# Performance work log

Hardware: AMD Instinct MI355X
Metric: run time of the kernel (lower is better)

## Reference

```python
import jax, jax.numpy as jnp
import numpy as np

T = 8192   # sequence length (= max_seq_len)
E = 1024   # embedding dim
D = 11     # hard-coded projection dim in source


def setup_inputs() -> dict:
    key = jax.random.key(0)
    ks = jax.random.split(key, 6)
    s_e = 1.0 / np.sqrt(E)
    s_d = 1.0 / np.sqrt(D)
    return {
        "x": jax.random.randint(ks[0], (T,), 0, 32000, dtype=jnp.int64),
        "x_embeddings": jax.random.normal(ks[1], (T, E), dtype=jnp.float32),
        "Wk": jax.random.normal(ks[2], (D, E), dtype=jnp.float32) * s_e,
        "bk": jnp.zeros((D,), dtype=jnp.float32),
        "Wq": jax.random.normal(ks[3], (D, E), dtype=jnp.float32) * s_e,
        "bq": jnp.zeros((D,), dtype=jnp.float32),
        "Wv": jax.random.normal(ks[4], (D, E), dtype=jnp.float32) * s_e,
        "bv": jnp.zeros((D,), dtype=jnp.float32),
        "Wf": jax.random.normal(ks[5], (E, D), dtype=jnp.float32) * s_d,
        "bf": jnp.zeros((E,), dtype=jnp.float32),
    }


def reference(x, x_embeddings, Wk, bk, Wq, bq, Wv, bv, Wf, bf):
    t = x.shape[0]  # static under jit
    k = x_embeddings @ Wk.T + bk            # [T, D]
    q = x_embeddings @ Wq.T + bq            # [T, D]
    v = x_embeddings @ Wv.T + bv            # [T, D]
    att = q @ k.T                           # [T, T]; NOTE: no 1/sqrt(D) scaling in source
    causal = jnp.tril(jnp.ones((t, t), dtype=bool))
    att = jnp.where(causal, att, -jnp.inf)
    att = jax.nn.softmax(att, axis=1)       # dim=1 as in source
    res = att @ v                           # [T, D]
    return res @ Wf.T + bf                  # [T, E]
```

## Files before the change

kernel.cpp:

```cpp
#include <hip/hip_runtime.h>

#define T_SEQ 8192
#define E_DIM 1024
#define QS 36
#define NEC 8
#define ECOLS 128
#define NC4 32
#define X4ST 33
#define RB 64
#define RPB 512
#define NIB (T_SEQ / RPB)
#define KVW 24
#define TR 16
#define LOG2E 1.4426950408889634f

__device__ __forceinline__ float2 pkfma(float2 a, float2 b, float2 c) {
    return make_float2(fmaf(a.x, b.x, c.x), fmaf(a.y, b.y, c.y));
}
__device__ __forceinline__ float2 f2(float x, float y) { return make_float2(x, y); }


__global__ __launch_bounds__(256) void prep_wf(const float* __restrict__ Wf,
                                               float* __restrict__ Wfp) {
    int id = blockIdx.x * 256 + threadIdx.x;
    if (id >= E_DIM * 12) return;
    int e = id / 12, d = id % 12;
    Wfp[id] = (d < 11) ? Wf[(size_t)e * 11 + d] : 0.f;
}

__global__ __launch_bounds__(256) void qkv_proj(
    const float* __restrict__ xe,
    const float* __restrict__ Wk, const float* __restrict__ bk,
    const float* __restrict__ Wq, const float* __restrict__ bq,
    const float* __restrict__ Wv, const float* __restrict__ bv,
    float* __restrict__ partQ) {
    const int row0 = blockIdx.x * RB;
    const int ec = blockIdx.y;
    const int lane = threadIdx.x & 63;
    const int wg = threadIdx.x >> 6;
    const int cb = ec * ECOLS;

    __shared__ float4 xT[RB * X4ST];
    __shared__ float4 wT[36 * NC4];

#pragma unroll
    for (int t = 0; t < 8; ++t) {
        int idx = threadIdx.x + t * 256;
        int r = idx >> 5, c4 = idx & 31;
        xT[r * X4ST + c4] =
            *(const float4*)(xe + (size_t)(row0 + r) * E_DIM + cb + c4 * 4);
    }
    for (int idx = threadIdx.x; idx < 36 * NC4; idx += 256) {
        int r = idx >> 5, c4 = idx & 31;
        float4 v = make_float4(0.f, 0.f, 0.f, 0.f);
        if (r < 33) {
            const float* base = (r < 11) ? (Wk + (size_t)r * E_DIM)
                              : (r < 22) ? (Wq + (size_t)(r - 11) * E_DIM)
                                         : (Wv + (size_t)(r - 22) * E_DIM);
            v = *(const float4*)(base + cb + c4 * 4);
        }
        wT[idx] = v;
    }
    __syncthreads();

    float2 acc[9];
#pragma unroll
    for (int k = 0; k < 9; ++k) acc[k] = f2(0.f, 0.f);

    const float4* xr = xT + lane * X4ST;
    const float4* wr = wT + wg * 9 * NC4;
#pragma unroll 4
    for (int c4 = 0; c4 < NC4; ++c4) {
        float4 xv = xr[c4];
        float2 xlo = f2(xv.x, xv.y), xhi = f2(xv.z, xv.w);
#pragma unroll
        for (int k = 0; k < 9; ++k) {
            float4 wv = wr[k * NC4 + c4];
            acc[k] = pkfma(xlo, f2(wv.x, wv.y), acc[k]);
            acc[k] = pkfma(xhi, f2(wv.z, wv.w), acc[k]);
        }
    }

    float* dst = partQ + ((size_t)ec * T_SEQ + row0 + lane) * QS;
#pragma unroll
    for (int k = 0; k < 9; ++k) {
        int o = wg * 9 + k;
        bool live = (o < 33);
        int c = (o < 11) ? o : (o < 22) ? o + 1 : (o < 33) ? o + 2
                : (o == 33) ? 11 : (o == 34) ? 23 : 35;
        float b = 0.f;
        if (ec == 0 && live)
            b = (o < 11) ? bk[o] : (o < 22) ? bq[o - 11] : bv[o - 22];
        dst[c] = live ? (acc[k].x + acc[k].y + b) : 0.f;
    }
}

__global__ __launch_bounds__(256) void reduceQ(const float* __restrict__ partQ,
                                               float* __restrict__ qkvF) {
    const size_t idx = (size_t)blockIdx.x * 256 + threadIdx.x;
    const float4* p = (const float4*)partQ;
    const size_t cs = (size_t)T_SEQ * (QS / 4);
    float4 s = make_float4(0.f, 0.f, 0.f, 0.f);
#pragma unroll
    for (int c = 0; c < NEC; ++c) {
        float4 a = p[idx + (size_t)c * cs];
        s.x += a.x; s.y += a.y; s.z += a.z; s.w += a.w;
    }
    ((float4*)qkvF)[idx] = s;
}

template <int LJCH>
__device__ __forceinline__ void stage_kv(const float* __restrict__ qkvF,
                                         float* kv, int j0) {
    for (int idx = threadIdx.x; idx < LJCH * 6; idx += 256) {
        int row = idx / 6, f = idx % 6;
        int srcOff = f * 4 + (f >= 3 ? 12 : 0);
        float4 v = *(const float4*)(qkvF + (size_t)(j0 + row) * QS + srcOff);
        *(float4*)(kv + row * KVW + f * 4) = v;
    }
}

template <int LJCH>
__device__ __forceinline__ void attn_chunk(const float* kv, int j0, int r0,
    const float4& qa0, const float4& qa1, const float4& qa2,
    const float4& qb0, const float4& qb1, const float4& qb2,
    float2& a01, float2& a23, float2& a45, float2& a67, float2& a89, float2& aXL,
    float2& b01, float2& b23, float2& b45, float2& b67, float2& b89, float2& bXL) {
#pragma unroll 2
    for (int jj = 0; jj < LJCH; ++jj) {
        const float* kp = kv + jj * KVW;
        const float4 kA = *(const float4*)(kp);
        const float4 kB = *(const float4*)(kp + 4);
        const float4 kC = *(const float4*)(kp + 8);
        const float4 vA = *(const float4*)(kp + 12);
        const float4 vB = *(const float4*)(kp + 16);
        const float4 vC = *(const float4*)(kp + 20);

        float2 sa = pkfma(f2(qa0.x, qa0.y), f2(kA.x, kA.y),
                    pkfma(f2(qa0.z, qa0.w), f2(kA.z, kA.w),
                    pkfma(f2(qa1.x, qa1.y), f2(kB.x, kB.y),
                    pkfma(f2(qa1.z, qa1.w), f2(kB.z, kB.w),
                    pkfma(f2(qa2.x, qa2.y), f2(kC.x, kC.y), f2(0.f, 0.f))))));
        float2 sb = pkfma(f2(qb0.x, qb0.y), f2(kA.x, kA.y),
                    pkfma(f2(qb0.z, qb0.w), f2(kA.z, kA.w),
                    pkfma(f2(qb1.x, qb1.y), f2(kB.x, kB.y),
                    pkfma(f2(qb1.z, qb1.w), f2(kB.z, kB.w),
                    pkfma(f2(qb2.x, qb2.y), f2(kC.x, kC.y), f2(0.f, 0.f))))));
        float pa = exp2f(sa.x + sa.y + qa2.z * kC.z);
        float pb = exp2f(sb.x + sb.y + qb2.z * kC.z);
        const int j = j0 + jj;
        pa = (j <= r0)     ? pa : 0.f;
        pb = (j <= r0 + 1) ? pb : 0.f;
        float2 pa2 = f2(pa, pa), pb2 = f2(pb, pb);
        a01 = pkfma(pa2, f2(vA.x, vA.y), a01);
        a23 = pkfma(pa2, f2(vA.z, vA.w), a23);
        a45 = pkfma(pa2, f2(vB.x, vB.y), a45);
        a67 = pkfma(pa2, f2(vB.z, vB.w), a67);
        a89 = pkfma(pa2, f2(vC.x, vC.y), a89);
        aXL = pkfma(pa2, f2(vC.z, 1.f),  aXL);
        b01 = pkfma(pb2, f2(vA.x, vA.y), b01);
        b23 = pkfma(pb2, f2(vA.z, vA.w), b23);
        b45 = pkfma(pb2, f2(vB.x, vB.y), b45);
        b67 = pkfma(pb2, f2(vB.z, vB.w), b67);
        b89 = pkfma(pb2, f2(vC.x, vC.y), b89);
        bXL = pkfma(pb2, f2(vC.z, 1.f),  bXL);
    }
}

template <int LJCH, int H>
__global__ __launch_bounds__(256, 4) void attn(const float* __restrict__ qkvF,
                                               float* __restrict__ part) {
    const int b = blockIdx.x;
    int ib = (int)((sqrtf((float)(8 * b / H + 1)) - 1.0f) * 0.5f);
    while (H * (ib + 1) * (ib + 2) / 2 <= b) ++ib;
    while (H * ib * (ib + 1) / 2 > b) --ib;
    const int s = b - H * ib * (ib + 1) / 2;
    const int chunkB = 2 * H * (ib + 1) - 1 - s;

    const int row0 = ib * RPB;
    const int r0 = row0 + threadIdx.x * 2;

    const float* qp0 = qkvF + (size_t)r0 * QS + 12;
    const float* qp1 = qp0 + QS;
    float4 qa0 = *(const float4*)(qp0), qa1 = *(const float4*)(qp0 + 4), qa2 = *(const float4*)(qp0 + 8);
    float4 qb0 = *(const float4*)(qp1), qb1 = *(const float4*)(qp1 + 4), qb2 = *(const float4*)(qp1 + 8);
    qa0.x *= LOG2E; qa0.y *= LOG2E; qa0.z *= LOG2E; qa0.w *= LOG2E;
    qa1.x *= LOG2E; qa1.y *= LOG2E; qa1.z *= LOG2E; qa1.w *= LOG2E;
    qa2.x *= LOG2E; qa2.y *= LOG2E; qa2.z *= LOG2E;
    qb0.x *= LOG2E; qb0.y *= LOG2E; qb0.z *= LOG2E; qb0.w *= LOG2E;
    qb1.x *= LOG2E; qb1.y *= LOG2E; qb1.z *= LOG2E; qb1.w *= LOG2E;
    qb2.x *= LOG2E; qb2.y *= LOG2E; qb2.z *= LOG2E;

    float2 a01 = f2(0.f, 0.f), a23 = a01, a45 = a01, a67 = a01, a89 = a01, aXL = a01;
    float2 b01 = a01, b23 = a01, b45 = a01, b67 = a01, b89 = a01, bXL = a01;

    __shared__ float kv[LJCH * KVW];

#pragma unroll
    for (int pass = 0; pass < 2; ++pass) {
        const int jc = pass ? chunkB : s;
        const int j0 = jc * LJCH;
        if (pass) __syncthreads();
        stage_kv<LJCH>(qkvF, kv, j0);
        __syncthreads();
        attn_chunk<LJCH>(kv, j0, r0, qa0, qa1, qa2, qb0, qb1, qb2,
                         a01, a23, a45, a67, a89, aXL, b01, b23, b45, b67, b89, bXL);
    }

    float* dst = part + ((size_t)s * T_SEQ + r0) * 12;
    float4 t;
    t.x = a01.x; t.y = a01.y; t.z = a23.x; t.w = a23.y; *(float4*)(dst + 0)  = t;
    t.x = a45.x; t.y = a45.y; t.z = a67.x; t.w = a67.y; *(float4*)(dst + 4)  = t;
    t.x = a89.x; t.y = a89.y; t.z = aXL.x; t.w = aXL.y; *(float4*)(dst + 8)  = t;
    t.x = b01.x; t.y = b01.y; t.z = b23.x; t.w = b23.y; *(float4*)(dst + 12) = t;
    t.x = b45.x; t.y = b45.y; t.z = b67.x; t.w = b67.y; *(float4*)(dst + 16) = t;
    t.x = b89.x; t.y = b89.y; t.z = bXL.x; t.w = bXL.y; *(float4*)(dst + 20) = t;
}

__global__ __launch_bounds__(256) void pass2(const float* __restrict__ part,
                                             const float* __restrict__ Wfp,
                                             const float* __restrict__ bf,
                                             float* __restrict__ out, int H) {
    const int t0 = blockIdx.x * TR;
    __shared__ float res[TR][12];
    const int cnt = H * (t0 / RPB) + H;
    if (threadIdx.x < TR * 12) {
        const float* p = part + (size_t)t0 * 12 + threadIdx.x;
        const size_t S = (size_t)T_SEQ * 12;
        float v[4];
#pragma unroll
        for (int u = 0; u < 4; ++u) v[u] = 0.f;
        for (int c = 0; c < cnt; c += 4) {
#pragma unroll
            for (int u = 0; u < 4; ++u) v[u] += p[(size_t)(c + u) * S];
        }
        float sum = (v[0] + v[1]) + (v[2] + v[3]);
        const int d = threadIdx.x % 12;
        res[threadIdx.x / 12][d] = (d == 11) ? (1.f / sum) : sum;
    }
    __syncthreads();

    const int e0 = threadIdx.x * 4;
    float4 wf[4][3];
#pragma unroll
    for (int ee = 0; ee < 4; ++ee) {
        const float4* wp = (const float4*)(Wfp + (size_t)(e0 + ee) * 12);
        wf[ee][0] = wp[0]; wf[ee][1] = wp[1]; wf[ee][2] = wp[2];
    }
    const float4 bv = *(const float4*)(bf + e0);

    for (int r = 0; r < TR; ++r) {
        float rr[12];
#pragma unroll
        for (int d = 0; d < 12; ++d) rr[d] = res[r][d];
        float2 a0 = f2(0.f, 0.f), a1 = a0, a2 = a0, a3 = a0;
#pragma unroll
        for (int d = 0; d < 10; d += 2) {
            float2 rv = f2(rr[d], rr[d + 1]);
            a0 = pkfma(rv, f2(((const float*)&wf[0][0])[d], ((const float*)&wf[0][0])[d + 1]), a0);
            a1 = pkfma(rv, f2(((const float*)&wf[1][0])[d], ((const float*)&wf[1][0])[d + 1]), a1);
            a2 = pkfma(rv, f2(((const float*)&wf[2][0])[d], ((const float*)&wf[2][0])[d + 1]), a2);
            a3 = pkfma(rv, f2(((const float*)&wf[3][0])[d], ((const float*)&wf[3][0])[d + 1]), a3);
        }
        const float rl = rr[11];
        float4 ov;
        ov.x = (a0.x + a0.y + rr[10] * wf[0][2].z) * rl + bv.x;
        ov.y = (a1.x + a1.y + rr[10] * wf[1][2].z) * rl + bv.y;
        ov.z = (a2.x + a2.y + rr[10] * wf[2][2].z) * rl + bv.z;
        ov.w = (a3.x + a3.y + rr[10] * wf[3][2].z) * rl + bv.w;
        *(float4*)(out + (size_t)(t0 + r) * E_DIM + e0) = ov;
    }
}

extern "C" void kernel_launch(void* const* d_in, const int* in_sizes, int n_in,
                              void* d_out, int out_size, void* d_ws, size_t ws_size,
                              hipStream_t stream) {
    const float* xe = (const float*)d_in[1];
    const float* Wk = (const float*)d_in[2];
    const float* bk = (const float*)d_in[3];
    const float* Wq = (const float*)d_in[4];
    const float* bq = (const float*)d_in[5];
    const float* Wv = (const float*)d_in[6];
    const float* bv = (const float*)d_in[7];
    const float* Wf = (const float*)d_in[8];
    const float* bf = (const float*)d_in[9];
    float* out = (float*)d_out;

    float* qkvF  = (float*)d_ws;
    float* wfp   = qkvF + (size_t)T_SEQ * QS;
    float* partQ = wfp + (size_t)E_DIM * 12;
    float* part  = partQ;

    const size_t fixed = ((size_t)T_SEQ * QS + (size_t)E_DIM * 12) * 4;
    const size_t need32 = fixed + (size_t)128 * T_SEQ * 12 * 4;

    prep_wf<<<(E_DIM * 12 + 255) / 256, 256, 0, stream>>>(Wf, wfp);
    qkv_proj<<<dim3(T_SEQ / RB, NEC), 256, 0, stream>>>(xe, Wk, bk, Wq, bq, Wv, bv, partQ);
    reduceQ<<<(T_SEQ * (QS / 4)) / 256, 256, 0, stream>>>(partQ, qkvF);

    if (ws_size >= need32) {
        attn<32, 8><<<8 * NIB * (NIB + 1) / 2, 256, 0, stream>>>(qkvF, part);
        pass2<<<T_SEQ / TR, 256, 0, stream>>>(part, wfp, bf, out, 8);
    } else {
        attn<64, 4><<<4 * NIB * (NIB + 1) / 2, 256, 0, stream>>>(qkvF, part);
        pass2<<<T_SEQ / TR, 256, 0, stream>>>(part, wfp, bf, out, 4);
    }
}
```

Measured before the change: 194.0 us.

## Register-block four rows per thread in QKV projection and causal attention

The QKV projection now has each thread compute four rows against a 64-column slice, using 16 column chunks. This reuses each shared-memory weight load across four rows. The attention kernel moves to 1024-row blocks with four query rows per thread and 64-key chunks, which reuses each K/V shared load four times, and it pads the kv stride. In exchange it uses more registers (launch bounds drop to 2 blocks per SM), launches fewer blocks, and removes the workspace-size fallback path.

```diff
diff --git a/kernel.cpp b/kernel.cpp
--- a/kernel.cpp
+++ b/kernel.cpp
@@ -3,14 +3,15 @@
 #define T_SEQ 8192
 #define E_DIM 1024
 #define QS 36
-#define NEC 8
-#define ECOLS 128
-#define NC4 32
-#define X4ST 33
-#define RB 64
-#define RPB 512
-#define NIB (T_SEQ / RPB)
-#define KVW 24
+#define QNEC 16
+#define QKC 64
+#define QX4 16
+#define QXST 17
+#define QRB 256
+#define AJC 64
+#define ARB 1024
+#define ANIB (T_SEQ / ARB)
+#define KVW 32
 #define TR 16
 #define LOG2E 1.4426950408889634f
 
@@ -28,30 +29,30 @@
     Wfp[id] = (d < 11) ? Wf[(size_t)e * 11 + d] : 0.f;
 }
 
-__global__ __launch_bounds__(256) void qkv_proj(
+__global__ __launch_bounds__(256, 2) void qkv_proj(
     const float* __restrict__ xe,
     const float* __restrict__ Wk, const float* __restrict__ bk,
     const float* __restrict__ Wq, const float* __restrict__ bq,
     const float* __restrict__ Wv, const float* __restrict__ bv,
     float* __restrict__ partQ) {
-    const int row0 = blockIdx.x * RB;
+    const int row0 = blockIdx.x * QRB;
     const int ec = blockIdx.y;
     const int lane = threadIdx.x & 63;
     const int wg = threadIdx.x >> 6;
-    const int cb = ec * ECOLS;
-
-    __shared__ float4 xT[RB * X4ST];
-    __shared__ float4 wT[36 * NC4];
-
-#pragma unroll
-    for (int t = 0; t < 8; ++t) {
+    const int cb = ec * QKC;
+
+    __shared__ float4 xT[QRB * QXST];
+    __shared__ float4 wT[36 * QX4];
+
+#pragma unroll
+    for (int t = 0; t < 16; ++t) {
         int idx = threadIdx.x + t * 256;
-        int r = idx >> 5, c4 = idx & 31;
-        xT[r * X4ST + c4] =
+        int r = idx >> 4, c4 = idx & 15;
+        xT[r * QXST + c4] =
             *(const float4*)(xe + (size_t)(row0 + r) * E_DIM + cb + c4 * 4);
     }
-    for (int idx = threadIdx.x; idx < 36 * NC4; idx += 256) {
-        int r = idx >> 5, c4 = idx & 31;
+    for (int idx = threadIdx.x; idx < 36 * QX4; idx += 256) {
+        int r = idx >> 4, c4 = idx & 15;
         float4 v = make_float4(0.f, 0.f, 0.f, 0.f);
         if (r < 33) {
             const float* base = (r < 11) ? (Wk + (size_t)r * E_DIM)
@@ -63,21 +64,32 @@
     }
     __syncthreads();
 
-    float2 acc[9];
-#pragma unroll
-    for (int k = 0; k < 9; ++k) acc[k] = f2(0.f, 0.f);
-
-    const float4* xr = xT + lane * X4ST;
-    const float4* wr = wT + wg * 9 * NC4;
+    float2 acc[4][9];
+#pragma unroll
+    for (int u = 0; u < 4; ++u)
+#pragma unroll
+        for (int k = 0; k < 9; ++k) acc[u][k] = f2(0.f, 0.f);
+
+    const float4* xr = xT + lane * QXST;
+    const float4* wr = wT + wg * 9 * QX4;
 #pragma unroll 4
-    for (int c4 = 0; c4 < NC4; ++c4) {
-        float4 xv = xr[c4];
-        float2 xlo = f2(xv.x, xv.y), xhi = f2(xv.z, xv.w);
+    for (int c4 = 0; c4 < QX4; ++c4) {
+        float4 xv0 = xr[c4];
+        float4 xv1 = xr[64 * QXST + c4];
+        float4 xv2 = xr[128 * QXST + c4];
+        float4 xv3 = xr[192 * QXST + c4];
 #pragma unroll
         for (int k = 0; k < 9; ++k) {
-            float4 wv = wr[k * NC4 + c4];
-            acc[k] = pkfma(xlo, f2(wv.x, wv.y), acc[k]);
-            acc[k] = pkfma(xhi, f2(wv.z, wv.w), acc[k]);
+            float4 wv = wr[k * QX4 + c4];
+            float2 wlo = f2(wv.x, wv.y), whi = f2(wv.z, wv.w);
+            acc[0][k] = pkfma(f2(xv0.x, xv0.y), wlo, acc[0][k]);
+            acc[0][k] = pkfma(f2(xv0.z, xv0.w), whi, acc[0][k]);
+            acc[1][k] = pkfma(f2(xv1.x, xv1.y), wlo, acc[1][k]);
+            acc[1][k] = pkfma(f2(xv1.z, xv1.w), whi, acc[1][k]);
+            acc[2][k] = pkfma(f2(xv2.x, xv2.y), wlo, acc[2][k]);
+            acc[2][k] = pkfma(f2(xv2.z, xv2.w), whi, acc[2][k]);
+            acc[3][k] = pkfma(f2(xv3.x, xv3.y), wlo, acc[3][k]);
+            acc[3][k] = pkfma(f2(xv3.z, xv3.w), whi, acc[3][k]);
         }
     }
 
@@ -87,11 +99,13 @@
         int o = wg * 9 + k;
         bool live = (o < 33);
         int c = (o < 11) ? o : (o < 22) ? o + 1 : (o < 33) ? o + 2
-                : (o == 33) ? 11 : (o == 34) ? 23 : 35;
+              : (o == 33) ? 11 : (o == 34) ? 23 : 35;
         float b = 0.f;
         if (ec == 0 && live)
             b = (o < 11) ? bk[o] : (o < 22) ? bq[o - 11] : bv[o - 22];
-        dst[c] = live ? (acc[k].x + acc[k].y + b) : 0.f;
+#pragma unroll
+        for (int u = 0; u < 4; ++u)
+            dst[(size_t)u * 64 * QS + c] = live ? (acc[u][k].x + acc[u][k].y + b) : 0.f;
     }
 }
 
@@ -102,128 +116,119 @@
     const size_t cs = (size_t)T_SEQ * (QS / 4);
     float4 s = make_float4(0.f, 0.f, 0.f, 0.f);
 #pragma unroll
-    for (int c = 0; c < NEC; ++c) {
+    for (int c = 0; c < QNEC; ++c) {
         float4 a = p[idx + (size_t)c * cs];
         s.x += a.x; s.y += a.y; s.z += a.z; s.w += a.w;
     }
     ((float4*)qkvF)[idx] = s;
 }
 
-template <int LJCH>
 __device__ __forceinline__ void stage_kv(const float* __restrict__ qkvF,
                                          float* kv, int j0) {
-    for (int idx = threadIdx.x; idx < LJCH * 6; idx += 256) {
-        int row = idx / 6, f = idx % 6;
-        int srcOff = f * 4 + (f >= 3 ? 12 : 0);
-        float4 v = *(const float4*)(qkvF + (size_t)(j0 + row) * QS + srcOff);
-        *(float4*)(kv + row * KVW + f * 4) = v;
-    }
-}
-
-template <int LJCH>
-__device__ __forceinline__ void attn_chunk(const float* kv, int j0, int r0,
-    const float4& qa0, const float4& qa1, const float4& qa2,
-    const float4& qb0, const float4& qb1, const float4& qb2,
-    float2& a01, float2& a23, float2& a45, float2& a67, float2& a89, float2& aXL,
-    float2& b01, float2& b23, float2& b45, float2& b67, float2& b89, float2& bXL) {
-#pragma unroll 2
-    for (int jj = 0; jj < LJCH; ++jj) {
-        const float* kp = kv + jj * KVW;
-        const float4 kA = *(const float4*)(kp);
-        const float4 kB = *(const float4*)(kp + 4);
-        const float4 kC = *(const float4*)(kp + 8);
-        const float4 vA = *(const float4*)(kp + 12);
-        const float4 vB = *(const float4*)(kp + 16);
-        const float4 vC = *(const float4*)(kp + 20);
-
-        float2 sa = pkfma(f2(qa0.x, qa0.y), f2(kA.x, kA.y),
-                    pkfma(f2(qa0.z, qa0.w), f2(kA.z, kA.w),
-                    pkfma(f2(qa1.x, qa1.y), f2(kB.x, kB.y),
-                    pkfma(f2(qa1.z, qa1.w), f2(kB.z, kB.w),
-                    pkfma(f2(qa2.x, qa2.y), f2(kC.x, kC.y), f2(0.f, 0.f))))));
-        float2 sb = pkfma(f2(qb0.x, qb0.y), f2(kA.x, kA.y),
-                    pkfma(f2(qb0.z, qb0.w), f2(kA.z, kA.w),
-                    pkfma(f2(qb1.x, qb1.y), f2(kB.x, kB.y),
-                    pkfma(f2(qb1.z, qb1.w), f2(kB.z, kB.w),
-                    pkfma(f2(qb2.x, qb2.y), f2(kC.x, kC.y), f2(0.f, 0.f))))));
-        float pa = exp2f(sa.x + sa.y + qa2.z * kC.z);
-        float pb = exp2f(sb.x + sb.y + qb2.z * kC.z);
-        const int j = j0 + jj;
-        pa = (j <= r0)     ? pa : 0.f;
-        pb = (j <= r0 + 1) ? pb : 0.f;
-        float2 pa2 = f2(pa, pa), pb2 = f2(pb, pb);
-        a01 = pkfma(pa2, f2(vA.x, vA.y), a01);
-        a23 = pkfma(pa2, f2(vA.z, vA.w), a23);
-        a45 = pkfma(pa2, f2(vB.x, vB.y), a45);
-        a67 = pkfma(pa2, f2(vB.z, vB.w), a67);
-        a89 = pkfma(pa2, f2(vC.x, vC.y), a89);
-        aXL = pkfma(pa2, f2(vC.z, 1.f),  aXL);
-        b01 = pkfma(pb2, f2(vA.x, vA.y), b01);
-        b23 = pkfma(pb2, f2(vA.z, vA.w), b23);
-        b45 = pkfma(pb2, f2(vB.x, vB.y), b45);
-        b67 = pkfma(pb2, f2(vB.z, vB.w), b67);
-        b89 = pkfma(pb2, f2(vC.x, vC.y), b89);
-        bXL = pkfma(pb2, f2(vC.z, 1.f),  bXL);
-    }
-}
-
-template <int LJCH, int H>
-__global__ __launch_bounds__(256, 4) void attn(const float* __restrict__ qkvF,
+    for (int idx = threadIdx.x; idx < AJC * 8; idx += 256) {
+        int row = idx >> 3, f = idx & 7;
+        if (f < 6) {
+            int srcOff = f * 4 + (f >= 3 ? 12 : 0);
+            float4 v = *(const float4*)(qkvF + (size_t)(j0 + row) * QS + srcOff);
+            *(float4*)(kv + row * KVW + f * 4) = v;
+        }
+    }
+}
+
+__global__ __launch_bounds__(256, 2) void attn(const float* __restrict__ qkvF,
                                                float* __restrict__ part) {
     const int b = blockIdx.x;
-    int ib = (int)((sqrtf((float)(8 * b / H + 1)) - 1.0f) * 0.5f);
-    while (H * (ib + 1) * (ib + 2) / 2 <= b) ++ib;
-    while (H * ib * (ib + 1) / 2 > b) --ib;
-    const int s = b - H * ib * (ib + 1) / 2;
-    const int chunkB = 2 * H * (ib + 1) - 1 - s;
-
-    const int row0 = ib * RPB;
-    const int r0 = row0 + threadIdx.x * 2;
-
-    const float* qp0 = qkvF + (size_t)r0 * QS + 12;
-    const float* qp1 = qp0 + QS;
-    float4 qa0 = *(const float4*)(qp0), qa1 = *(const float4*)(qp0 + 4), qa2 = *(const float4*)(qp0 + 8);
-    float4 qb0 = *(const float4*)(qp1), qb1 = *(const float4*)(qp1 + 4), qb2 = *(const float4*)(qp1 + 8);
-    qa0.x *= LOG2E; qa0.y *= LOG2E; qa0.z *= LOG2E; qa0.w *= LOG2E;
-    qa1.x *= LOG2E; qa1.y *= LOG2E; qa1.z *= LOG2E; qa1.w *= LOG2E;
-    qa2.x *= LOG2E; qa2.y *= LOG2E; qa2.z *= LOG2E;
-    qb0.x *= LOG2E; qb0.y *= LOG2E; qb0.z *= LOG2E; qb0.w *= LOG2E;
-    qb1.x *= LOG2E; qb1.y *= LOG2E; qb1.z *= LOG2E; qb1.w *= LOG2E;
-    qb2.x *= LOG2E; qb2.y *= LOG2E; qb2.z *= LOG2E;
-
-    float2 a01 = f2(0.f, 0.f), a23 = a01, a45 = a01, a67 = a01, a89 = a01, aXL = a01;
-    float2 b01 = a01, b23 = a01, b45 = a01, b67 = a01, b89 = a01, bXL = a01;
-
-    __shared__ float kv[LJCH * KVW];
+    int ib = 0;
+    while (4 * (ib + 1) * (ib + 2) <= b) ++ib;
+    const int s = b - 4 * ib * (ib + 1);
+    const int C = 16 * (ib + 1);
+
+    const int rbase = ib * ARB + threadIdx.x * 4;
+
+    float2 q[4][6];
+#pragma unroll
+    for (int u = 0; u < 4; ++u) {
+        const float* qp = qkvF + (size_t)(rbase + u) * QS + 12;
+#pragma unroll
+        for (int d = 0; d < 5; ++d)
+            q[u][d] = f2(qp[2 * d] * LOG2E, qp[2 * d + 1] * LOG2E);
+        q[u][5] = f2(qp[10] * LOG2E, 0.f);
+    }
+
+    float2 acc[4][6];
+#pragma unroll
+    for (int u = 0; u < 4; ++u)
+#pragma unroll
+        for (int d = 0; d < 6; ++d) acc[u][d] = f2(0.f, 0.f);
+
+    __shared__ float kv[AJC * KVW];
 
 #pragma unroll
     for (int pass = 0; pass < 2; ++pass) {
-        const int jc = pass ? chunkB : s;
-        const int j0 = jc * LJCH;
+        const int jc = pass ? (C - 1 - s) : s;
+        const int j0 = jc * AJC;
         if (pass) __syncthreads();
-        stage_kv<LJCH>(qkvF, kv, j0);
+        stage_kv(qkvF, kv, j0);
         __syncthreads();
-        attn_chunk<LJCH>(kv, j0, r0, qa0, qa1, qa2, qb0, qb1, qb2,
-                         a01, a23, a45, a67, a89, aXL, b01, b23, b45, b67, b89, bXL);
-    }
-
-    float* dst = part + ((size_t)s * T_SEQ + r0) * 12;
-    float4 t;
-    t.x = a01.x; t.y = a01.y; t.z = a23.x; t.w = a23.y; *(float4*)(dst + 0)  = t;
-    t.x = a45.x; t.y = a45.y; t.z = a67.x; t.w = a67.y; *(float4*)(dst + 4)  = t;
-    t.x = a89.x; t.y = a89.y; t.z = aXL.x; t.w = aXL.y; *(float4*)(dst + 8)  = t;
-    t.x = b01.x; t.y = b01.y; t.z = b23.x; t.w = b23.y; *(float4*)(dst + 12) = t;
-    t.x = b45.x; t.y = b45.y; t.z = b67.x; t.w = b67.y; *(float4*)(dst + 16) = t;
-    t.x = b89.x; t.y = b89.y; t.z = bXL.x; t.w = bXL.y; *(float4*)(dst + 20) = t;
+
+        for (int jj = 0; jj < AJC; ++jj) {
+            const float* kp = kv + jj * KVW;
+            const float4 kA = *(const float4*)(kp);
+            const float4 kB = *(const float4*)(kp + 4);
+            const float4 kC = *(const float4*)(kp + 8);
+            const float4 vA = *(const float4*)(kp + 12);
+            const float4 vB = *(const float4*)(kp + 16);
+            const float4 vC = *(const float4*)(kp + 20);
+            const float2 k01 = f2(kA.x, kA.y), k23 = f2(kA.z, kA.w);
+            const float2 k45 = f2(kB.x, kB.y), k67 = f2(kB.z, kB.w);
+            const float2 k89 = f2(kC.x, kC.y), kXp = f2(kC.z, kC.w);
+            const int j = j0 + jj;
+
+            float p[4];
+#pragma unroll
+            for (int u = 0; u < 4; ++u) {
+                float2 sv = pkfma(q[u][0], k01,
+                            pkfma(q[u][1], k23,
+                            pkfma(q[u][2], k45,
+                            pkfma(q[u][3], k67,
+                            pkfma(q[u][4], k89,
+                            pkfma(q[u][5], kXp, f2(0.f, 0.f)))))));
+                float e = exp2f(sv.x + sv.y);
+                p[u] = (j <= rbase + u) ? e : 0.f;
+            }
+#pragma unroll
+            for (int u = 0; u < 4; ++u) {
+                float2 p2 = f2(p[u], p[u]);
+                acc[u][0] = pkfma(p2, f2(vA.x, vA.y), acc[u][0]);
+                acc[u][1] = pkfma(p2, f2(vA.z, vA.w), acc[u][1]);
+                acc[u][2] = pkfma(p2, f2(vB.x, vB.y), acc[u][2]);
+                acc[u][3] = pkfma(p2, f2(vB.z, vB.w), acc[u][3]);
+                acc[u][4] = pkfma(p2, f2(vC.x, vC.y), acc[u][4]);
+                acc[u][5] = pkfma(p2, f2(vC.z, 1.f), acc[u][5]);
+            }
+        }
+    }
+
+#pragma unroll
+    for (int u = 0; u < 4; ++u) {
+        float* dst = part + ((size_t)s * T_SEQ + rbase + u) * 12;
+        float4 t;
+        t.x = acc[u][0].x; t.y = acc[u][0].y; t.z = acc[u][1].x; t.w = acc[u][1].y;
+        *(float4*)(dst + 0) = t;
+        t.x = acc[u][2].x; t.y = acc[u][2].y; t.z = acc[u][3].x; t.w = acc[u][3].y;
+        *(float4*)(dst + 4) = t;
+        t.x = acc[u][4].x; t.y = acc[u][4].y; t.z = acc[u][5].x; t.w = acc[u][5].y;
+        *(float4*)(dst + 8) = t;
+    }
 }
 
 __global__ __launch_bounds__(256) void pass2(const float* __restrict__ part,
                                              const float* __restrict__ Wfp,
                                              const float* __restrict__ bf,
-                                             float* __restrict__ out, int H) {
+                                             float* __restrict__ out) {
     const int t0 = blockIdx.x * TR;
     __shared__ float res[TR][12];
-    const int cnt = H * (t0 / RPB) + H;
+    const int cnt = 8 * (t0 / ARB) + 8;
     if (threadIdx.x < TR * 12) {
         const float* p = part + (size_t)t0 * 12 + threadIdx.x;
         const size_t S = (size_t)T_SEQ * 12;
@@ -291,18 +296,9 @@
     float* partQ = wfp + (size_t)E_DIM * 12;
     float* part  = partQ;
 
-    const size_t fixed = ((size_t)T_SEQ * QS + (size_t)E_DIM * 12) * 4;
-    const size_t need32 = fixed + (size_t)128 * T_SEQ * 12 * 4;
-
     prep_wf<<<(E_DIM * 12 + 255) / 256, 256, 0, stream>>>(Wf, wfp);
-    qkv_proj<<<dim3(T_SEQ / RB, NEC), 256, 0, stream>>>(xe, Wk, bk, Wq, bq, Wv, bv, partQ);
+    qkv_proj<<<dim3(T_SEQ / QRB, QNEC), 256, 0, stream>>>(xe, Wk, bk, Wq, bq, Wv, bv, partQ);
     reduceQ<<<(T_SEQ * (QS / 4)) / 256, 256, 0, stream>>>(partQ, qkvF);
-
-    if (ws_size >= need32) {
-        attn<32, 8><<<8 * NIB * (NIB + 1) / 2, 256, 0, stream>>>(qkvF, part);
-        pass2<<<T_SEQ / TR, 256, 0, stream>>>(part, wfp, bf, out, 8);
-    } else {
-        attn<64, 4><<<4 * NIB * (NIB + 1) / 2, 256, 0, stream>>>(qkvF, part);
-        pass2<<<T_SEQ / TR, 256, 0, stream>>>(part, wfp, bf, out, 4);
-    }
-}
+    attn<<<4 * ANIB * (ANIB + 1), 256, 0, stream>>>(qkvF, part);
+    pass2<<<T_SEQ / TR, 256, 0, stream>>>(part, wfp, bf, out);
+}
```

Result: slower. 223.3 us (+15.1%).
